# Kernel tuning notes

Hardware: AMD Instinct MI355X
Metric: run time of the kernel (lower is better)

The kernel has to match this reference:

```python
import jax, jax.numpy as jnp
import numpy as np

B, T, D, H = 8, 2048, 1024, 128

def setup_inputs() -> dict:
    key = jax.random.key(0)
    ks = jax.random.split(key, 8)
    s = 1.0 / np.sqrt(D)
    return {
        "x": jax.random.normal(ks[0], (B, T, D), dtype=jnp.float32),
        "att": jax.random.normal(ks[1], (B, T, D), dtype=jnp.float32),
        "Wk": jax.random.uniform(ks[2], (D, H), minval=-s, maxval=s, dtype=jnp.float32),
        "bk": jax.random.uniform(ks[3], (H,), minval=-s, maxval=s, dtype=jnp.float32),
        "Wq": jax.random.uniform(ks[4], (D, H), minval=-s, maxval=s, dtype=jnp.float32),
        "bq": jax.random.uniform(ks[5], (H,), minval=-s, maxval=s, dtype=jnp.float32),
        "Wv": jax.random.uniform(ks[6], (D, H), minval=-s, maxval=s, dtype=jnp.float32),
        "bv": jax.random.uniform(ks[7], (H,), minval=-s, maxval=s, dtype=jnp.float32),
    }

def reference(x, att, Wk, bk, Wq, bq, Wv, bv):
    # k, q from `att`; v from `x` (as in the original module)
    k = jnp.einsum('btd,dh->bth', att, Wk) + bk   # [B,T,H]
    q = jnp.einsum('btd,dh->bth', att, Wq) + bq   # [B,T,H]
    v = jnp.einsum('btd,dh->bth', x, Wv) + bv     # [B,T,H]
    # Faithful to source: scores / head_size**(-0.5) == scores * sqrt(head_size)
    scale = jnp.asarray(k.shape[-1], jnp.float32) ** 0.5
    scores = jnp.einsum('bqh,bkh->bqk', q, k) * scale  # [B,T,T]
    att_mat = jax.nn.softmax(scores, axis=-1)
    # dropout p=0.0 -> identity (eval semantics)
    return jnp.einsum('bqk,bkh->bqh', att_mat, v)      # [B,T,H]
```

## Files before the change

### kernel.cpp

```cpp
#include <hip/hip_runtime.h>
#include <stdint.h>

typedef unsigned short u16;
typedef __attribute__((ext_vector_type(8))) short bf16x8;
typedef __attribute__((ext_vector_type(4))) float f32x4;

#define T_LEN 2048
#define D_DIM 1024
#define H_DIM 128
#define SCALE_LOG2 16.32223116f

#define EXP2F(x) __builtin_amdgcn_exp2f(x)

__device__ __forceinline__ u16 f2bf(float f) {
  uint32_t u = __float_as_uint(f);
  u += 0x7FFFu + ((u >> 16) & 1u);
  return (u16)(u >> 16);
}
__device__ __forceinline__ float bf2f(u16 h) { return __uint_as_float(((uint32_t)h) << 16); }

__device__ __forceinline__ void gload16(const void* g, void* l) {
  __builtin_amdgcn_global_load_lds(
      (const __attribute__((address_space(1))) uint32_t*)(uintptr_t)g,
      (__attribute__((address_space(3))) uint32_t*)(uint32_t)(uintptr_t)l,
      16, 0, 0);
}

#define VMCNT0() asm volatile("s_waitcnt vmcnt(0)" ::: "memory")
#define VMLG0() asm volatile("s_waitcnt vmcnt(0) lgkmcnt(0)" ::: "memory")
#define BAR() __builtin_amdgcn_s_barrier()
#define PRIO(n) __builtin_amdgcn_s_setprio(n)

#define MFMA(a, b, c) __builtin_amdgcn_mfma_f32_16x16x32_bf16((a), (b), (c), 0, 0, 0)

__global__ __launch_bounds__(256) void prep_w(
    const float* __restrict__ Wk, const float* __restrict__ Wq, const float* __restrict__ Wv,
    u16* __restrict__ wqh, u16* __restrict__ wql,
    u16* __restrict__ wkh, u16* __restrict__ wkl,
    u16* __restrict__ wvh) {
  __shared__ u16 th[3][128][16];
  __shared__ u16 tl[2][128][16];
  const int i = threadIdx.x;
  const int d0 = blockIdx.x * 16;
  const int dl = i >> 4;
  const int hb = (i & 15) * 8;
  const int d = d0 + dl;
#pragma unroll
  for (int e = 0; e < 8; ++e) {
    int h = hb + e;
    float q = Wq[d * H_DIM + h] * SCALE_LOG2;
    float k = Wk[d * H_DIM + h];
    float v = Wv[d * H_DIM + h];
    u16 qh = f2bf(q); th[0][h][dl] = qh; tl[0][h][dl] = f2bf(q - bf2f(qh));
    u16 kh = f2bf(k); th[1][h][dl] = kh; tl[1][h][dl] = f2bf(k - bf2f(kh));
    th[2][h][dl] = f2bf(v);
  }
  __syncthreads();
  const int h = i >> 1, c = i & 1;
  u16* planes[5] = {wqh, wql, wkh, wkl, wvh};
  const u16* srcs[5] = {&th[0][0][0], &tl[0][0][0], &th[1][0][0], &tl[1][0][0], &th[2][0][0]};
#pragma unroll
  for (int p = 0; p < 5; ++p) {
    bf16x8 v8 = *(const bf16x8*)(srcs[p] + h * 16 + c * 8);
    *(bf16x8*)(planes[p] + h * 1024 + d0 + c * 8) = v8;
  }
}

#define QBUF 53248

__global__ __launch_bounds__(512) void qkv_proj(
    const float* __restrict__ att, const float* __restrict__ x,
    const u16* __restrict__ wqh, const u16* __restrict__ wql,
    const u16* __restrict__ wkh, const u16* __restrict__ wkl,
    const u16* __restrict__ wvh,
    const float* __restrict__ bq, const float* __restrict__ bk, const float* __restrict__ bv,
    u16* __restrict__ qhp, u16* __restrict__ qlp,
    u16* __restrict__ khp, u16* __restrict__ klp,
    u16* __restrict__ vtp) {
  __shared__ __attribute__((aligned(128))) char lds[104 * 1024];

  const int tid = threadIdx.x;
  const int wid = tid >> 6;
  const int ln = tid & 63;
  const int g = ln >> 4;
  const int cl = ln & 15;
  const int t0g = blockIdx.x * 64;

  const f32x4 fz = {0.f, 0.f, 0.f, 0.f};
  f32x4 accq[4], acck[4], accv[4];
#pragma unroll
  for (int s = 0; s < 4; ++s) { accq[s] = fz; acck[s] = fz; accv[s] = fz; }

  const int isA = tid < 256;
  const int at = tid & 255;
  const int arow = at >> 2;
  const int ac = at & 3;
  const float* srcp = (isA ? att : x) + (size_t)(t0g + arow) * D_DIM + ac * 8;
  const int aw_off = (isA ? 0 : 8192) + arow * 64 + ((ac ^ ((arow >> 1) & 3)) * 16);

  auto STAGE_W = [&](int b, int ks) {
    char* wt = lds + b * QBUF + 12288;
#pragma unroll
    for (int j = 0; j < 5; ++j) {
      int seg = wid * 5 + j;
      int p = seg >> 3;
      int s = seg & 7;
      int db = s * 1024 + ln * 16;
      int row = db >> 6;
      int c = (db >> 4) & 3;
      int cs = c ^ ((row >> 1) & 3);
      const u16* wp = (p == 0) ? wqh : (p == 1) ? wql : (p == 2) ? wkh : (p == 3) ? wkl : wvh;
      gload16(wp + row * 1024 + ks * 32 + cs * 8, wt + p * 8192 + s * 1024);
    }
  };
  auto CWRITE_A = [&](int b, f32x4 f0, f32x4 f1) {
    bf16x8 vh, vl;
#pragma unroll
    for (int e = 0; e < 4; ++e) {
      u16 h0 = f2bf(f0[e]); vh[e] = (short)h0; vl[e] = (short)f2bf(f0[e] - bf2f(h0));
      u16 h1 = f2bf(f1[e]); vh[e + 4] = (short)h1; vl[e + 4] = (short)f2bf(f1[e] - bf2f(h1));
    }
    char* dst = lds + b * QBUF + aw_off;
    *(bf16x8*)dst = vh;
    if (isA) *(bf16x8*)(dst + 4096) = vl;
  };

  {
    f32x4 f0 = *(const f32x4*)(srcp);
    f32x4 f1 = *(const f32x4*)(srcp + 4);
    STAGE_W(0, 0);
    CWRITE_A(0, f0, f1);
  }
  VMLG0();
  BAR();

  int cur = 0;
  for (int ks = 0; ks < 32; ++ks) {
    f32x4 pf0, pf1;
    if (ks < 31) {
      pf0 = *(const f32x4*)(srcp + (ks + 1) * 32);
      pf1 = *(const f32x4*)(srcp + (ks + 1) * 32 + 4);
      STAGE_W(cur ^ 1, ks + 1);
    }
    char* base = lds + cur * QBUF;
    char* wt = base + 12288;
    bf16x8 ah[4], al[4], xh[4];
#pragma unroll
    for (int s = 0; s < 4; ++s) {
      int row = s * 16 + cl;
      int byte = row * 64 + ((g ^ ((row >> 1) & 3)) * 16);
      ah[s] = *(const bf16x8*)(base + byte);
      al[s] = *(const bf16x8*)(base + 4096 + byte);
      xh[s] = *(const bf16x8*)(base + 8192 + byte);
    }
    {
      int hrow = wid * 16 + cl;
      int wb = hrow * 64 + ((g ^ ((hrow >> 1) & 3)) * 16);
      bf16x8 bqh_ = *(const bf16x8*)(wt + 0 * 8192 + wb);
      bf16x8 bql_ = *(const bf16x8*)(wt + 1 * 8192 + wb);
      bf16x8 bkh_ = *(const bf16x8*)(wt + 2 * 8192 + wb);
      bf16x8 bkl_ = *(const bf16x8*)(wt + 3 * 8192 + wb);
      bf16x8 bvh_ = *(const bf16x8*)(wt + 4 * 8192 + wb);
      PRIO(1);
#pragma unroll
      for (int s = 0; s < 4; ++s) {
        accq[s] = MFMA(ah[s], bqh_, accq[s]);
        accq[s] = MFMA(al[s], bqh_, accq[s]);
        accq[s] = MFMA(ah[s], bql_, accq[s]);
        acck[s] = MFMA(ah[s], bkh_, acck[s]);
        acck[s] = MFMA(al[s], bkh_, acck[s]);
        acck[s] = MFMA(ah[s], bkl_, acck[s]);
        accv[s] = MFMA(xh[s], bvh_, accv[s]);
      }
      PRIO(0);
    }
    if (ks < 31) CWRITE_A(cur ^ 1, pf0, pf1);
    VMLG0();
    BAR();
    cur ^= 1;
  }

  char* vbuf = lds;
  {
    int h = wid * 16 + cl;
    float bqv = bq[h] * SCALE_LOG2, bkv = bk[h], bvv = bv[h];
#pragma unroll
    for (int s = 0; s < 4; ++s) {
#pragma unroll
      for (int r = 0; r < 4; ++r) {
        int t = s * 16 + g * 4 + r;
        size_t idx = (size_t)(t0g + t) * H_DIM + h;
        float qv = accq[s][r] + bqv;
        u16 qh_ = f2bf(qv);
        qhp[idx] = qh_;
        qlp[idx] = f2bf(qv - bf2f(qh_));
        float kv = acck[s][r] + bkv;
        u16 kh_ = f2bf(kv);
        khp[idx] = kh_;
        klp[idx] = f2bf(kv - bf2f(kh_));
        float vv = accv[s][r] + bvv;
        int c3 = t >> 3;
        int byte = h * 128 + ((c3 ^ (h & 7)) * 16) + (t & 7) * 2;
        *(u16*)(vbuf + byte) = f2bf(vv);
      }
    }
  }
  __syncthreads();
  {
    int h = tid >> 2, qtr = tid & 3;
    int b2 = t0g >> 11;
    int tb = t0g & 2047;
    u16* dst = vtp + ((size_t)(b2 * H_DIM + h)) * T_LEN + tb + qtr * 16;
#pragma unroll
    for (int c2 = 0; c2 < 2; ++c2) {
      int c3 = qtr * 2 + c2;
      bf16x8 v8 = *(const bf16x8*)(vbuf + h * 128 + ((c3 ^ (h & 7)) * 16));
      *(bf16x8*)(dst + c2 * 8) = v8;
    }
  }
}

#define KVB 32
#define GBUF 24576

__global__ __launch_bounds__(512) void attn(
    const u16* __restrict__ qhp, const u16* __restrict__ qlp,
    const u16* __restrict__ khp, const u16* __restrict__ klp,
    const u16* __restrict__ vtp,
    float* __restrict__ out) {
  __shared__ __attribute__((aligned(128))) char lds[104 * 1024];

  const int tid = threadIdx.x;
  const int wid = tid >> 6;
  const int w4 = wid & 3;
  const int gb = wid >> 2;
  const int ln = tid & 63;
  const int g = ln >> 4;
  const int cl = ln & 15;
  const int bid = blockIdx.x;
  const int b_ = bid & 7;
  const int t0 = (bid >> 3) * 64;
  char* gl = lds + gb * 2 * GBUF;
  char* pW = lds + 96 * 1024 + wid * 1024;

  auto STAGE = [&](int cb, int tk) {
    char* base = gl + cb * GBUF;
#pragma unroll
    for (int j = 0; j < 6; ++j) {
      int seg = w4 * 6 + j;
      int p = seg >> 3;
      int s = seg & 7;
      int db = s * 1024 + ln * 16;
      if (p < 2) {
        int row = db >> 8;
        int c16 = (db >> 4) & 15;
        int cs = c16 ^ (row & 7);
        size_t gidx = (size_t)(b_ * T_LEN + tk + row) * H_DIM + cs * 8;
        gload16((p ? klp : khp) + gidx, base + p * 8192 + s * 1024);
      } else {
        int vrow = db >> 6;
        int c = (db >> 4) & 3;
        int vcs = c ^ (vrow & 3);
        size_t vidx = (size_t)(b_ * H_DIM + vrow) * T_LEN + tk + vcs * 8;
        gload16(vtp + vidx, base + 16384 + s * 1024);
      }
    }
  };

  bf16x8 qh_f[4], ql_f[4];
  {
    size_t qrow = (size_t)(b_ * T_LEN + t0 + w4 * 16 + cl) * H_DIM;
#pragma unroll
    for (int kc = 0; kc < 4; ++kc) {
      qh_f[kc] = *(const bf16x8*)(qhp + qrow + kc * 32 + g * 8);
      ql_f[kc] = *(const bf16x8*)(qlp + qrow + kc * 32 + g * 8);
    }
  }
  const f32x4 fz = {0.f, 0.f, 0.f, 0.f};
  float m_[4] = {-1e30f, -1e30f, -1e30f, -1e30f};
  float l_[4] = {0.f, 0.f, 0.f, 0.f};
  f32x4 o_[8];
#pragma unroll
  for (int ht = 0; ht < 8; ++ht) o_[ht] = fz;

  const int tkbase = gb * 1024;

  STAGE(0, tkbase);
  VMCNT0();
  BAR();

  int cur = 0;
  for (int kv = 0; kv < 32; ++kv) {
    if (kv < 31) STAGE(cur ^ 1, tkbase + (kv + 1) * KVB);

    char* kH = gl + cur * GBUF;
    char* kL = kH + 8192;
    char* vT = kH + 16384;
    f32x4 sc[2] = {fz, fz};
    PRIO(1);
#pragma unroll
    for (int kc = 0; kc < 4; ++kc) {
#pragma unroll
      for (int nt = 0; nt < 2; ++nt) {
        int row = nt * 16 + cl;
        int byte = row * 256 + (((kc * 4 + g) ^ (row & 7)) * 16);
        bf16x8 bh = *(const bf16x8*)(kH + byte);
        bf16x8 bl = *(const bf16x8*)(kL + byte);
        sc[nt] = MFMA(qh_f[kc], bh, sc[nt]);
        sc[nt] = MFMA(ql_f[kc], bh, sc[nt]);
        sc[nt] = MFMA(qh_f[kc], bl, sc[nt]);
      }
    }
    PRIO(0);
    float sfv[4];
#pragma unroll
    for (int r = 0; r < 4; ++r) {
      float pm = fmaxf(sc[0][r], sc[1][r]);
#pragma unroll
      for (int d = 1; d < 16; d <<= 1) pm = fmaxf(pm, __shfl_xor(pm, d));
      float mn = fmaxf(m_[r], pm);
      float sf = EXP2F(m_[r] - mn);
      m_[r] = mn; sfv[r] = sf;
      float ps = 0.f;
      int prow = g * 4 + r;
#pragma unroll
      for (int nt = 0; nt < 2; ++nt) {
        float p = EXP2F(sc[nt][r] - mn);
        ps += p;
        int c3 = nt * 2 + (cl >> 3);
        int byte = prow * 64 + ((c3 ^ (prow & 3)) * 16) + (cl & 7) * 2;
        *(u16*)(pW + byte) = f2bf(p);
      }
#pragma unroll
      for (int d = 1; d < 16; d <<= 1) ps += __shfl_xor(ps, d);
      l_[r] = l_[r] * sf + ps;
    }
#pragma unroll
    for (int ht = 0; ht < 8; ++ht) {
      o_[ht][0] *= sfv[0]; o_[ht][1] *= sfv[1]; o_[ht][2] *= sfv[2]; o_[ht][3] *= sfv[3];
    }
    {
      int pbyte = cl * 64 + ((g ^ (cl & 3)) * 16);
      bf16x8 ap = *(const bf16x8*)(pW + pbyte);
      PRIO(1);
#pragma unroll
      for (int ht = 0; ht < 8; ++ht) {
        int vrow = ht * 16 + cl;
        int vbyte = vrow * 64 + ((g ^ (vrow & 3)) * 16);
        bf16x8 bv_ = *(const bf16x8*)(vT + vbyte);
        o_[ht] = MFMA(ap, bv_, o_[ht]);
      }
      PRIO(0);
    }
    VMCNT0();
    BAR();
    cur ^= 1;
  }

  if (gb == 1) {
    char* ob = lds + w4 * 8192 + ln * 128;
#pragma unroll
    for (int ht = 0; ht < 8; ++ht) *(f32x4*)(ob + ht * 16) = o_[ht];
    f32x4 mv = {m_[0], m_[1], m_[2], m_[3]};
    f32x4 lv = {l_[0], l_[1], l_[2], l_[3]};
    char* mb = lds + 32768 + w4 * 2048 + ln * 32;
    *(f32x4*)mb = mv;
    *(f32x4*)(mb + 16) = lv;
  }
  __syncthreads();
  if (gb == 0) {
    char* ob = lds + w4 * 8192 + ln * 128;
    char* mb = lds + 32768 + w4 * 2048 + ln * 32;
    f32x4 mB = *(const f32x4*)mb;
    f32x4 lB = *(const f32x4*)(mb + 16);
    float sA[4], sB[4];
#pragma unroll
    for (int r = 0; r < 4; ++r) {
      float m = fmaxf(m_[r], mB[r]);
      float fa = EXP2F(m_[r] - m);
      float fb = EXP2F(mB[r] - m);
      float inv = 1.f / (l_[r] * fa + lB[r] * fb);
      sA[r] = fa * inv;
      sB[r] = fb * inv;
    }
    size_t obase = (size_t)(b_ * T_LEN + t0 + w4 * 16) * H_DIM;
#pragma unroll
    for (int ht = 0; ht < 8; ++ht) {
      f32x4 oB = *(const f32x4*)(ob + ht * 16);
#pragma unroll
      for (int r = 0; r < 4; ++r) {
        out[obase + (size_t)(g * 4 + r) * H_DIM + ht * 16 + cl] =
            o_[ht][r] * sA[r] + oB[r] * sB[r];
      }
    }
  }
}

extern "C" void kernel_launch(void* const* d_in, const int* in_sizes, int n_in,
                              void* d_out, int out_size, void* d_ws, size_t ws_size,
                              hipStream_t stream) {
  const float* x   = (const float*)d_in[0];
  const float* att = (const float*)d_in[1];
  const float* Wk  = (const float*)d_in[2];
  const float* bk  = (const float*)d_in[3];
  const float* Wq  = (const float*)d_in[4];
  const float* bq  = (const float*)d_in[5];
  const float* Wv  = (const float*)d_in[6];
  const float* bv  = (const float*)d_in[7];
  float* out = (float*)d_out;
  char* ws = (char*)d_ws;

  u16* wqh = (u16*)(ws);
  u16* wql = (u16*)(ws + 256 * 1024);
  u16* wkh = (u16*)(ws + 512 * 1024);
  u16* wkl = (u16*)(ws + 768 * 1024);
  u16* wvh = (u16*)(ws + 1024 * 1024);
  u16* qhp = (u16*)(ws + (size_t)2 * 1024 * 1024);
  u16* qlp = (u16*)(ws + (size_t)6 * 1024 * 1024);
  u16* khp = (u16*)(ws + (size_t)10 * 1024 * 1024);
  u16* klp = (u16*)(ws + (size_t)14 * 1024 * 1024);
  u16* vtp = (u16*)(ws + (size_t)18 * 1024 * 1024);

  prep_w<<<64, 256, 0, stream>>>(Wk, Wq, Wv, wqh, wql, wkh, wkl, wvh);
  qkv_proj<<<256, 512, 0, stream>>>(att, x, wqh, wql, wkh, wkl, wvh,
                                    bq, bk, bv, qhp, qlp, khp, klp, vtp);
  attn<<<256, 512, 0, stream>>>(qhp, qlp, khp, klp, vtp, out);
}
```

Baseline: 262.1 us.

## Rewrite attention kernel with 32x32 MFMA, register P, and lazy rescaling

The attention kernel moves to 32x32x16 bf16 MFMAs with transposed S (K as the A operand). The P fragment now stays in registers via cvt_pk and permlane32 swap, replacing the LDS round trip. V is read straight from global memory into registers, K hi/lo tiles are staged through LDS with register prefetch, and the block shrinks to 4 waves with lower LDS use. Online-softmax rescaling is skipped unless the max grows by more than 8 (log2 units), which cuts VALU work but leaves direct global V loads uncached in LDS and exposed to latency.

```diff
diff --git a/kernel.cpp b/kernel.cpp
--- a/kernel.cpp
+++ b/kernel.cpp
@@ -4,6 +4,9 @@
 typedef unsigned short u16;
 typedef __attribute__((ext_vector_type(8))) short bf16x8;
 typedef __attribute__((ext_vector_type(4))) float f32x4;
+typedef __attribute__((ext_vector_type(16))) float f32x16;
+typedef __attribute__((ext_vector_type(4))) uint32_t u32x4;
+typedef __attribute__((ext_vector_type(2))) int int2v;
 
 #define T_LEN 2048
 #define D_DIM 1024
@@ -28,10 +31,32 @@
 
 #define VMCNT0() asm volatile("s_waitcnt vmcnt(0)" ::: "memory")
 #define VMLG0() asm volatile("s_waitcnt vmcnt(0) lgkmcnt(0)" ::: "memory")
+#define LGKM0() asm volatile("s_waitcnt lgkmcnt(0)" ::: "memory")
 #define BAR() __builtin_amdgcn_s_barrier()
 #define PRIO(n) __builtin_amdgcn_s_setprio(n)
 
 #define MFMA(a, b, c) __builtin_amdgcn_mfma_f32_16x16x32_bf16((a), (b), (c), 0, 0, 0)
+#define MFMA32(a, b, c) __builtin_amdgcn_mfma_f32_32x32x16_bf16((a), (b), (c), 0, 0, 0)
+
+__device__ __forceinline__ uint32_t cvtpk(float lo, float hi) {
+  uint32_t r;
+  asm("v_cvt_pk_bf16_f32 %0, %1, %2" : "=v"(r) : "v"(lo), "v"(hi));
+  return r;
+}
+__device__ __forceinline__ void plswap(uint32_t& a, uint32_t& b, int hi) {
+#if __has_builtin(__builtin_amdgcn_permlane32_swap)
+  int2v r = __builtin_amdgcn_permlane32_swap((int)a, (int)b, false, false);
+  a = (uint32_t)r.x;
+  b = (uint32_t)r.y;
+#else
+  uint32_t as = (uint32_t)__shfl_xor((int)a, 32);
+  uint32_t bs = (uint32_t)__shfl_xor((int)b, 32);
+  uint32_t na = hi ? bs : a;
+  uint32_t nb = hi ? b : as;
+  a = na;
+  b = nb;
+#endif
+}
 
 __global__ __launch_bounds__(256) void prep_w(
     const float* __restrict__ Wk, const float* __restrict__ Wq, const float* __restrict__ Wv,
@@ -220,177 +245,176 @@
   }
 }
 
-#define KVB 32
-#define GBUF 24576
-
-__global__ __launch_bounds__(512) void attn(
+#define NTILES 32
+
+__global__ __launch_bounds__(256, 1) void attn(
     const u16* __restrict__ qhp, const u16* __restrict__ qlp,
     const u16* __restrict__ khp, const u16* __restrict__ klp,
     const u16* __restrict__ vtp,
     float* __restrict__ out) {
-  __shared__ __attribute__((aligned(128))) char lds[104 * 1024];
+  __shared__ __attribute__((aligned(128))) char lds[33 * 1024];
 
   const int tid = threadIdx.x;
-  const int wid = tid >> 6;
-  const int w4 = wid & 3;
-  const int gb = wid >> 2;
-  const int ln = tid & 63;
-  const int g = ln >> 4;
-  const int cl = ln & 15;
+  const int w = tid >> 6;
+  const int l = tid & 63;
+  const int q5 = l & 31;
+  const int hi = l >> 5;
   const int bid = blockIdx.x;
   const int b_ = bid & 7;
   const int t0 = (bid >> 3) * 64;
-  char* gl = lds + gb * 2 * GBUF;
-  char* pW = lds + 96 * 1024 + wid * 1024;
-
-  auto STAGE = [&](int cb, int tk) {
-    char* base = gl + cb * GBUF;
-#pragma unroll
-    for (int j = 0; j < 6; ++j) {
-      int seg = w4 * 6 + j;
-      int p = seg >> 3;
-      int s = seg & 7;
-      int db = s * 1024 + ln * 16;
-      if (p < 2) {
-        int row = db >> 8;
-        int c16 = (db >> 4) & 15;
-        int cs = c16 ^ (row & 7);
-        size_t gidx = (size_t)(b_ * T_LEN + tk + row) * H_DIM + cs * 8;
-        gload16((p ? klp : khp) + gidx, base + p * 8192 + s * 1024);
-      } else {
-        int vrow = db >> 6;
-        int c = (db >> 4) & 3;
-        int vcs = c ^ (vrow & 3);
-        size_t vidx = (size_t)(b_ * H_DIM + vrow) * T_LEN + tk + vcs * 8;
-        gload16(vtp + vidx, base + 16384 + s * 1024);
+  const int wq = w >> 1;
+  const int kvh = w & 1;
+  const int qrow = t0 + wq * 32 + q5;
+  const int tkb = kvh * 1024;
+
+  bf16x8 qh[8], ql[8];
+  {
+    const u16* qb = qhp + ((size_t)(b_ * T_LEN + qrow)) * H_DIM + hi * 8;
+    const u16* qlb = qlp + ((size_t)(b_ * T_LEN + qrow)) * H_DIM + hi * 8;
+#pragma unroll
+    for (int kc = 0; kc < 8; ++kc) {
+      qh[kc] = *(const bf16x8*)(qb + kc * 16);
+      ql[kc] = *(const bf16x8*)(qlb + kc * 16);
+    }
+  }
+
+  uint32_t goff[8], ldsoff[8];
+#pragma unroll
+  for (int i = 0; i < 8; ++i) {
+    int gid = i * 256 + tid;
+    int half = gid >> 10;
+    int plane = (gid >> 9) & 1;
+    int n = gid & 511;
+    int row = n >> 4;
+    int slot = n & 15;
+    int dg = slot ^ (row & 15);
+    goff[i] = (uint32_t)(plane * 2097152 +
+                         (b_ * T_LEN + half * 1024 + row) * H_DIM + dg * 8);
+    ldsoff[i] = (uint32_t)(gid * 16);
+  }
+
+  f32x16 o[4] = {};
+  float m_ = -1e30f;
+  float l_ = 0.f;
+
+  int4 st[8];
+#pragma unroll
+  for (int i = 0; i < 8; ++i) st[i] = *(const int4*)(khp + goff[i]);
+#pragma unroll
+  for (int i = 0; i < 8; ++i) *(int4*)(lds + ldsoff[i]) = st[i];
+  __syncthreads();
+
+  for (int t = 0; t < NTILES; ++t) {
+    if (t < NTILES - 1) {
+#pragma unroll
+      for (int i = 0; i < 8; ++i)
+        st[i] = *(const int4*)(khp + goff[i] + (t + 1) * 4096);
+    }
+    bf16x8 vfr[8];
+#pragma unroll
+    for (int ks = 0; ks < 2; ++ks)
+#pragma unroll
+      for (int nt = 0; nt < 4; ++nt)
+        vfr[ks * 4 + nt] = *(const bf16x8*)(
+            vtp + ((size_t)(b_ * H_DIM + nt * 32 + q5)) * T_LEN +
+            tkb + t * 32 + ks * 16 + hi * 8);
+
+    f32x16 s = {};
+#pragma unroll
+    for (int kc = 0; kc < 8; ++kc) {
+      int slot = (kc * 2 + hi) ^ (q5 & 15);
+      const char* kb = lds + kvh * 16384 + q5 * 256 + slot * 16;
+      bf16x8 kh_f = *(const bf16x8*)(kb);
+      bf16x8 kl_f = *(const bf16x8*)(kb + 8192);
+      s = MFMA32(kh_f, qh[kc], s);
+      s = MFMA32(kl_f, qh[kc], s);
+      s = MFMA32(kh_f, ql[kc], s);
+    }
+
+    float pmax = s[0];
+#pragma unroll
+    for (int j = 1; j < 16; ++j) pmax = fmaxf(pmax, s[j]);
+    pmax = fmaxf(pmax, __shfl_xor(pmax, 32));
+    if (__any(pmax > m_ + 8.f)) {
+      float mn = fmaxf(m_, pmax);
+      float sf = EXP2F(m_ - mn);
+      m_ = mn;
+      l_ *= sf;
+#pragma unroll
+      for (int j = 0; j < 16; ++j) {
+        int rj = (j & 3) + 8 * (j >> 2) + 4 * hi;
+        float sfj = __shfl(sf, rj);
+        o[0][j] *= sfj; o[1][j] *= sfj; o[2][j] *= sfj; o[3][j] *= sfj;
       }
     }
-  };
-
-  bf16x8 qh_f[4], ql_f[4];
-  {
-    size_t qrow = (size_t)(b_ * T_LEN + t0 + w4 * 16 + cl) * H_DIM;
-#pragma unroll
-    for (int kc = 0; kc < 4; ++kc) {
-      qh_f[kc] = *(const bf16x8*)(qhp + qrow + kc * 32 + g * 8);
-      ql_f[kc] = *(const bf16x8*)(qlp + qrow + kc * 32 + g * 8);
-    }
-  }
-  const f32x4 fz = {0.f, 0.f, 0.f, 0.f};
-  float m_[4] = {-1e30f, -1e30f, -1e30f, -1e30f};
-  float l_[4] = {0.f, 0.f, 0.f, 0.f};
-  f32x4 o_[8];
-#pragma unroll
-  for (int ht = 0; ht < 8; ++ht) o_[ht] = fz;
-
-  const int tkbase = gb * 1024;
-
-  STAGE(0, tkbase);
-  VMCNT0();
-  BAR();
-
-  int cur = 0;
-  for (int kv = 0; kv < 32; ++kv) {
-    if (kv < 31) STAGE(cur ^ 1, tkbase + (kv + 1) * KVB);
-
-    char* kH = gl + cur * GBUF;
-    char* kL = kH + 8192;
-    char* vT = kH + 16384;
-    f32x4 sc[2] = {fz, fz};
-    PRIO(1);
-#pragma unroll
-    for (int kc = 0; kc < 4; ++kc) {
-#pragma unroll
-      for (int nt = 0; nt < 2; ++nt) {
-        int row = nt * 16 + cl;
-        int byte = row * 256 + (((kc * 4 + g) ^ (row & 7)) * 16);
-        bf16x8 bh = *(const bf16x8*)(kH + byte);
-        bf16x8 bl = *(const bf16x8*)(kL + byte);
-        sc[nt] = MFMA(qh_f[kc], bh, sc[nt]);
-        sc[nt] = MFMA(ql_f[kc], bh, sc[nt]);
-        sc[nt] = MFMA(qh_f[kc], bl, sc[nt]);
-      }
-    }
-    PRIO(0);
-    float sfv[4];
-#pragma unroll
-    for (int r = 0; r < 4; ++r) {
-      float pm = fmaxf(sc[0][r], sc[1][r]);
-#pragma unroll
-      for (int d = 1; d < 16; d <<= 1) pm = fmaxf(pm, __shfl_xor(pm, d));
-      float mn = fmaxf(m_[r], pm);
-      float sf = EXP2F(m_[r] - mn);
-      m_[r] = mn; sfv[r] = sf;
-      float ps = 0.f;
-      int prow = g * 4 + r;
-#pragma unroll
-      for (int nt = 0; nt < 2; ++nt) {
-        float p = EXP2F(sc[nt][r] - mn);
-        ps += p;
-        int c3 = nt * 2 + (cl >> 3);
-        int byte = prow * 64 + ((c3 ^ (prow & 3)) * 16) + (cl & 7) * 2;
-        *(u16*)(pW + byte) = f2bf(p);
-      }
-#pragma unroll
-      for (int d = 1; d < 16; d <<= 1) ps += __shfl_xor(ps, d);
-      l_[r] = l_[r] * sf + ps;
-    }
-#pragma unroll
-    for (int ht = 0; ht < 8; ++ht) {
-      o_[ht][0] *= sfv[0]; o_[ht][1] *= sfv[1]; o_[ht][2] *= sfv[2]; o_[ht][3] *= sfv[3];
-    }
-    {
-      int pbyte = cl * 64 + ((g ^ (cl & 3)) * 16);
-      bf16x8 ap = *(const bf16x8*)(pW + pbyte);
-      PRIO(1);
-#pragma unroll
-      for (int ht = 0; ht < 8; ++ht) {
-        int vrow = ht * 16 + cl;
-        int vbyte = vrow * 64 + ((g ^ (vrow & 3)) * 16);
-        bf16x8 bv_ = *(const bf16x8*)(vT + vbyte);
-        o_[ht] = MFMA(ap, bv_, o_[ht]);
-      }
-      PRIO(0);
-    }
-    VMCNT0();
+    float p[16];
+#pragma unroll
+    for (int j = 0; j < 16; ++j) p[j] = EXP2F(s[j] - m_);
+    float ps = 0.f;
+#pragma unroll
+    for (int j = 0; j < 16; ++j) ps += p[j];
+    ps += __shfl_xor(ps, 32);
+    l_ += ps;
+
+    uint32_t u0 = cvtpk(p[0], p[1]), v0 = cvtpk(p[4], p[5]);
+    uint32_t u1 = cvtpk(p[2], p[3]), v1 = cvtpk(p[6], p[7]);
+    uint32_t u2 = cvtpk(p[8], p[9]), v2 = cvtpk(p[12], p[13]);
+    uint32_t u3 = cvtpk(p[10], p[11]), v3 = cvtpk(p[14], p[15]);
+    plswap(u0, v0, hi);
+    plswap(u1, v1, hi);
+    plswap(u2, v2, hi);
+    plswap(u3, v3, hi);
+    u32x4 f0w = {u0, u1, v0, v1};
+    u32x4 f1w = {u2, u3, v2, v3};
+    bf16x8 pa0 = *(bf16x8*)&f0w;
+    bf16x8 pa1 = *(bf16x8*)&f1w;
+
+#pragma unroll
+    for (int nt = 0; nt < 4; ++nt) o[nt] = MFMA32(pa0, vfr[nt], o[nt]);
+#pragma unroll
+    for (int nt = 0; nt < 4; ++nt) o[nt] = MFMA32(pa1, vfr[4 + nt], o[nt]);
+
+    LGKM0();
     BAR();
-    cur ^= 1;
-  }
-
-  if (gb == 1) {
-    char* ob = lds + w4 * 8192 + ln * 128;
-#pragma unroll
-    for (int ht = 0; ht < 8; ++ht) *(f32x4*)(ob + ht * 16) = o_[ht];
-    f32x4 mv = {m_[0], m_[1], m_[2], m_[3]};
-    f32x4 lv = {l_[0], l_[1], l_[2], l_[3]};
-    char* mb = lds + 32768 + w4 * 2048 + ln * 32;
-    *(f32x4*)mb = mv;
-    *(f32x4*)(mb + 16) = lv;
-  }
+    if (t < NTILES - 1) {
+#pragma unroll
+      for (int i = 0; i < 8; ++i) *(int4*)(lds + ldsoff[i]) = st[i];
+    }
+    LGKM0();
+    BAR();
+  }
+
   __syncthreads();
-  if (gb == 0) {
-    char* ob = lds + w4 * 8192 + ln * 128;
-    char* mb = lds + 32768 + w4 * 2048 + ln * 32;
-    f32x4 mB = *(const f32x4*)mb;
-    f32x4 lB = *(const f32x4*)(mb + 16);
-    float sA[4], sB[4];
-#pragma unroll
-    for (int r = 0; r < 4; ++r) {
-      float m = fmaxf(m_[r], mB[r]);
-      float fa = EXP2F(m_[r] - m);
-      float fb = EXP2F(mB[r] - m);
-      float inv = 1.f / (l_[r] * fa + lB[r] * fb);
-      sA[r] = fa * inv;
-      sB[r] = fb * inv;
-    }
-    size_t obase = (size_t)(b_ * T_LEN + t0 + w4 * 16) * H_DIM;
-#pragma unroll
-    for (int ht = 0; ht < 8; ++ht) {
-      f32x4 oB = *(const f32x4*)(ob + ht * 16);
-#pragma unroll
-      for (int r = 0; r < 4; ++r) {
-        out[obase + (size_t)(g * 4 + r) * H_DIM + ht * 16 + cl] =
-            o_[ht][r] * sA[r] + oB[r] * sB[r];
+  if (kvh == 1) {
+    float* ob = (float*)(lds + wq * 16384);
+#pragma unroll
+    for (int nt = 0; nt < 4; ++nt)
+#pragma unroll
+      for (int j = 0; j < 16; ++j) ob[nt * 1024 + j * 64 + l] = o[nt][j];
+    if (hi == 0) {
+      float* mlb = (float*)(lds + 32768 + wq * 256);
+      mlb[q5 * 2] = m_;
+      mlb[q5 * 2 + 1] = l_;
+    }
+  }
+  __syncthreads();
+  if (kvh == 0) {
+    float* ob = (float*)(lds + wq * 16384);
+    float* mlb = (float*)(lds + 32768 + wq * 256);
+    float mB = mlb[q5 * 2], lB = mlb[q5 * 2 + 1];
+    float mM = fmaxf(m_, mB);
+    float fa = EXP2F(m_ - mM), fb = EXP2F(mB - mM);
+    float inv = 1.f / (l_ * fa + lB * fb);
+    float sA = fa * inv, sB = fb * inv;
+#pragma unroll
+    for (int j = 0; j < 16; ++j) {
+      int rj = (j & 3) + 8 * (j >> 2) + 4 * hi;
+      float sAj = __shfl(sA, rj);
+      float sBj = __shfl(sB, rj);
+      size_t rbase = ((size_t)(b_ * T_LEN + t0 + wq * 32 + rj)) * H_DIM + q5;
+#pragma unroll
+      for (int nt = 0; nt < 4; ++nt) {
+        out[rbase + nt * 32] = o[nt][j] * sAj + ob[nt * 1024 + j * 64 + l] * sBj;
       }
     }
   }
@@ -424,5 +448,5 @@
   prep_w<<<64, 256, 0, stream>>>(Wk, Wq, Wv, wqh, wql, wkh, wkl, wvh);
   qkv_proj<<<256, 512, 0, stream>>>(att, x, wqh, wql, wkh, wkl, wvh,
                                     bq, bk, bv, qhp, qlp, khp, klp, vtp);
-  attn<<<256, 512, 0, stream>>>(qhp, qlp, khp, klp, vtp, out);
-}
+  attn<<<256, 256, 0, stream>>>(qhp, qlp, khp, klp, vtp, out);
+}
```

After: 331.6 us. 1.27x slower.
